# Kernel optimization log

Measured on AMD Instinct MI355X. Metric: run time of the kernel, lower is better.

Reference implementation:

```python
import jax, jax.numpy as jnp
import numpy as np

B, L, DIM, H, D, WS = 2, 2048, 1024, 16, 64, 256
SCALE = D ** -0.5


def _rope_tables(seq_len, dim, dtype):
    inv_freq = 1.0 / (10000.0 ** (jnp.arange(0, dim, 2, dtype=jnp.float32) / dim))
    t = jnp.arange(seq_len, dtype=jnp.float32)
    freqs = jnp.einsum('i,j->ij', t, inv_freq)          # [L, D/2]
    emb = jnp.concatenate([freqs, freqs], axis=-1)       # [L, D]
    return jnp.cos(emb).astype(dtype), jnp.sin(emb).astype(dtype)


def _rotate_half(x):
    x1, x2 = x[..., : x.shape[-1] // 2], x[..., x.shape[-1] // 2:]
    return jnp.concatenate([-x2, x1], axis=-1)


def _apply_rope(t, cos, sin):
    # t: [B, L, H, D]; cos/sin: [L, D] broadcast over batch and heads
    return t * cos[None, :, None, :] + _rotate_half(t) * sin[None, :, None, :]


def setup_inputs() -> dict:
    key = jax.random.key(0)
    k0, k1, k2 = jax.random.split(key, 3)
    x = jax.random.normal(k0, (B, L, DIM), dtype=jnp.float32)
    Wqkv = jax.random.normal(k1, (3 * H * D, DIM), dtype=jnp.float32) * 0.02
    bqkv = jnp.zeros((3 * H * D,), dtype=jnp.float32)
    Wproj = jax.random.normal(k2, (DIM, H * D), dtype=jnp.float32) * 0.02
    bproj = jnp.zeros((DIM,), dtype=jnp.float32)
    return {"x": x, "Wqkv": Wqkv, "bqkv": bqkv, "Wproj": Wproj, "bproj": bproj, "is_global": 1}


def _attention(x, Wqkv, bqkv, Wproj, bproj, is_global):
    b, l, _ = x.shape
    qkv = x @ Wqkv.T + bqkv                              # [B, L, 3*H*D]
    q, k, v = jnp.split(qkv, 3, axis=-1)
    q, k, v = (t.reshape(b, l, H, D) for t in (q, k, v))
    cos, sin = _rope_tables(l, D, x.dtype)
    q = _apply_rope(q, cos, sin)
    k = _apply_rope(k, cos, sin)
    if is_global:
        attn = jnp.einsum('bshd,bthd->bhst', q, k) * SCALE
        attn = jax.nn.softmax(attn, axis=-1)
        out = jnp.einsum('bhst,bthd->bshd', attn, v)     # [B, L, H, D]
    else:
        pad = (WS - l % WS) % WS
        if pad > 0:
            q, k, v = (jnp.pad(t, ((0, 0), (0, pad), (0, 0), (0, 0))) for t in (q, k, v))
        w = (l + pad) // WS
        q = q.reshape(b, w, WS, H, D)
        k = k.reshape(b, w, WS, H, D)
        v = v.reshape(b, w, WS, H, D)
        attn = jnp.einsum('bwshd,bwthd->bwhst', q, k) * SCALE
        attn = jax.nn.softmax(attn, axis=-1)
        out = jnp.einsum('bwhst,bwthd->bwshd', attn, v).reshape(b, w * WS, H, D)
        out = out[:, :l]
    return out.reshape(b, l, H * D) @ Wproj.T + bproj


def reference(x, Wqkv, bqkv, Wproj, bproj, is_global):
    return _attention(x, Wqkv, bqkv, Wproj, bproj, is_global)
```

## Files before the change

### kernel.cpp

```cpp
#include <hip/hip_runtime.h>
#include <math.h>

#define NB 2
#define NL 2048
#define NDIM 1024
#define NH 16
#define ND 64
#define NWS 256
#define NM (NB*NL)
#define QSCALE 0.18033688011112042f

typedef __attribute__((ext_vector_type(8))) short short8;
typedef __attribute__((ext_vector_type(4))) float f32x4;
typedef unsigned short ushort_t;
typedef unsigned int uint_t;

#define MFMA16(a,b,acc) __builtin_amdgcn_mfma_f32_16x16x32_bf16((a),(b),(acc),0,0,0)

static __device__ __forceinline__ ushort_t f2bf(float x){
    uint_t u = __float_as_uint(x);
    uint_t r = (u + 0x7fff + ((u >> 16) & 1)) >> 16;
    return (ushort_t)r;
}
static __device__ __forceinline__ float bf2f(ushort_t u){
    return __uint_as_float(((uint_t)u) << 16);
}
static __device__ __forceinline__ float fast_exp2(float x){
#if __has_builtin(__builtin_amdgcn_exp2f)
    return __builtin_amdgcn_exp2f(x);
#else
    return exp2f(x);
#endif
}

static __device__ __forceinline__ void async_load16(const void* g, void* l){
    __builtin_amdgcn_global_load_lds(
        (const __attribute__((address_space(1))) unsigned int*)g,
        (__attribute__((address_space(3))) unsigned int*)l, 16, 0, 0);
}

__launch_bounds__(256)
__global__ void split_all(const float* __restrict__ x,  ushort_t* __restrict__ xh,  ushort_t* __restrict__ xl,
                          const float* __restrict__ wq, ushort_t* __restrict__ wqh, ushort_t* __restrict__ wql,
                          const float* __restrict__ wp, ushort_t* __restrict__ wph, ushort_t* __restrict__ wpl)
{
    int i = blockIdx.x*256 + threadIdx.x;
    const float* in; ushort_t *oh, *ol;
    if (i < 1048576)      { in = x;  oh = xh;  ol = xl;  }
    else if (i < 1835008) { in = wq; oh = wqh; ol = wql; i -= 1048576; }
    else                  { in = wp; oh = wph; ol = wpl; i -= 1835008; }
    const int e = i*4;
    const float4 v = *(const float4*)(in + e);
    ushort_t h0=f2bf(v.x), h1=f2bf(v.y), h2=f2bf(v.z), h3=f2bf(v.w);
    ushort4 h4; h4.x=h0; h4.y=h1; h4.z=h2; h4.w=h3;
    ushort4 l4;
    l4.x=f2bf(v.x - bf2f(h0)); l4.y=f2bf(v.y - bf2f(h1));
    l4.z=f2bf(v.z - bf2f(h2)); l4.w=f2bf(v.w - bf2f(h3));
    *(ushort4*)(oh + e) = h4;
    *(ushort4*)(ol + e) = l4;
}

__launch_bounds__(256)
__global__ void rope_tab(float* __restrict__ tc, float* __restrict__ ts)
{
    const int idx = blockIdx.x*256 + threadIdx.x;
    const int j = idx >> 11, l = idx & (NL-1);
    const float invf = 1.0f / powf(10000.0f, (float)j * (1.0f/32.0f));
    float s, c;
    sincosf((float)l * invf, &s, &c);
    tc[idx] = c; ts[idx] = s;
}

template<int MODE>
__launch_bounds__(256, 3)
__global__ void gemm_hl(const ushort_t* __restrict__ Ah, const ushort_t* __restrict__ Al,
                        const ushort_t* __restrict__ Bh, const ushort_t* __restrict__ Bl,
                        const float* __restrict__ bias,
                        float* __restrict__ Cout,
                        ushort_t* __restrict__ oQh, ushort_t* __restrict__ oKh,
                        ushort_t* __restrict__ oVth,
                        const float* __restrict__ tcos, const float* __restrict__ tsin)
{
    __shared__ __align__(16) char smem[50176];
    ushort_t* sA_h = (ushort_t*)smem;
    ushort_t* sA_l = (ushort_t*)(smem + 8192);
    ushort_t* sB_h = (ushort_t*)(smem + 16384);
    ushort_t* sB_l = (ushort_t*)(smem + 20480);
    ushort_t* sBounce = (ushort_t*)smem;
    const int ebuf = 12288;
    const int bbuf = 24576;
    const int NTILE = (MODE==0) ? 128 : 64;
    const int WN    = (MODE==0) ? 64  : 32;
    const int NTT   = (MODE==0) ? 4   : 2;

    const int tid  = threadIdx.x;
    const int wv   = tid >> 6, lane = tid & 63;
    const int quad = lane >> 4, l16 = lane & 15;
    const int m0 = blockIdx.y << 7, n0 = blockIdx.x * NTILE;
    const int wr = wv >> 1, wc = wv & 1;

    const ushort_t* gsrc;
    ushort_t* lds_base;
    int rowb, npass;
    if (MODE == 1) {
        gsrc = (wv==0)?Ah:(wv==1)?Al:(wv==2)?Bh:Bl;
        lds_base = (wv==0)?sA_h:(wv==1)?sA_l:(wv==2)?sB_h:sB_l;
        rowb = (wv < 2) ? m0 : n0;
        npass = (wv < 2) ? 8 : 4;
    } else {
        if (wv == 0)      { gsrc = Ah; lds_base = sA_h; rowb = m0; npass = 8; }
        else if (wv == 1) { gsrc = Al; lds_base = sA_l; rowb = m0; npass = 8; }
        else { gsrc = Bh; lds_base = sB_h + (wv-2)*64*32; rowb = n0 + (wv-2)*64; npass = 4; }
    }
    const int rl = lane >> 2;
    const int cp = lane & 3;
    const int cg = cp ^ ((rl >> 1) & 3);
    const ushort_t* gptr = gsrc + (size_t)(rowb + rl)*NDIM + cg*8;

    f32x4 acc[4][NTT];
    #pragma unroll
    for (int i=0;i<4;++i)
        #pragma unroll
        for (int j=0;j<NTT;++j) acc[i][j] = (f32x4){0.f,0.f,0.f,0.f};

    const int swz = (l16 >> 1) & 3;
    const int ac_off = (wr*64 + l16)*32 + ((quad ^ swz) << 3);
    const int bc_off = (wc*WN + l16)*32 + ((quad ^ swz) << 3);

#define GSTAGE(BUF, KOFF) do { \
        const ushort_t* gp_ = gptr + (KOFF); \
        for (int p=0; p<npass; ++p) \
            async_load16(gp_ + (size_t)p*16*NDIM, (char*)lds_base + (BUF)*bbuf + p*1024); \
    } while(0)

#define GCOMP(BUF) do { \
        const int eo_ = (BUF)*ebuf; \
        short8 ah[4], al[4], bh[NTT], bl[NTT]; \
        _Pragma("unroll") \
        for (int t=0;t<4;++t){ \
            ah[t] = *(const short8*)&sA_h[eo_ + t*512 + ac_off]; \
            al[t] = *(const short8*)&sA_l[eo_ + t*512 + ac_off]; \
        } \
        _Pragma("unroll") \
        for (int t=0;t<NTT;++t){ \
            bh[t] = *(const short8*)&sB_h[eo_ + t*512 + bc_off]; \
            if (MODE == 1) bl[t] = *(const short8*)&sB_l[eo_ + t*512 + bc_off]; \
        } \
        _Pragma("unroll") \
        for (int mt=0;mt<4;++mt) \
            _Pragma("unroll") \
            for (int nt=0;nt<NTT;++nt){ \
                f32x4 a_ = acc[mt][nt]; \
                a_ = MFMA16(ah[mt], bh[nt], a_); \
                a_ = MFMA16(al[mt], bh[nt], a_); \
                if (MODE == 1) a_ = MFMA16(ah[mt], bl[nt], a_); \
                acc[mt][nt] = a_; \
            } \
    } while(0)

    GSTAGE(0, 0);
    for (int k0 = 0; k0 < NDIM; k0 += 64) {
        __syncthreads();
        GSTAGE(1, k0 + 32);
        GCOMP(0);
        __syncthreads();
        if (k0 + 64 < NDIM) GSTAGE(0, k0 + 64);
        GCOMP(1);
    }
#undef GSTAGE
#undef GCOMP

    if (MODE == 1) {
        const int colb = n0 + wc*32;
        float bq[2];
        #pragma unroll
        for (int nt=0;nt<2;++nt) bq[nt] = bias[colb + nt*16 + l16];
        #pragma unroll
        for (int mt=0;mt<4;++mt)
            #pragma unroll
            for (int r=0;r<4;++r){
                const int m = m0 + wr*64 + mt*16 + quad*4 + r;
                float* orow = Cout + (size_t)m*NDIM + colb;
                #pragma unroll
                for (int nt=0;nt<2;++nt)
                    orow[nt*16 + l16] = acc[mt][nt][r] + bq[nt];
            }
    } else {
        const int colb = n0 + wc*64;
        const int sel  = colb >> 10;
        const int head = (colb & 1023) >> 6;
        float bq[4];
        #pragma unroll
        for (int nt=0;nt<4;++nt) bq[nt] = bias[colb + nt*16 + l16];

        if (sel == 2) {
            __syncthreads();
            const int bb = m0 >> 11;
            const int Lb = (m0 & (NL-1)) + wr*64;
            ushort_t* sT = sBounce + wv*(64*72);
            const size_t gb = ((size_t)(bb*NH + head)*ND)*NL + Lb;
            const int drow = lane >> 3, dcol = lane & 7;
            #pragma unroll
            for (int mt=0;mt<4;++mt)
                #pragma unroll
                for (int nt=0;nt<4;++nt)
                    #pragma unroll
                    for (int r=0;r<4;++r)
                        sT[(nt*16+l16)*72 + mt*16 + quad*4 + r] = f2bf(acc[mt][nt][r] + bq[nt]);
            #pragma unroll
            for (int dd=0; dd<8; ++dd){
                const int d = dd*8 + drow;
                const uint4 v = *(const uint4*)&sT[d*72 + dcol*8];
                *(uint4*)(oVth + gb + (size_t)d*NL + dcol*8) = v;
            }
        } else {
            ushort_t* dh = sel ? oKh : oQh;
            const float qs = sel ? 1.0f : QSCALE;
            #pragma unroll
            for (int mt=0;mt<4;++mt)
                #pragma unroll
                for (int r=0;r<4;++r){
                    const int m = m0 + wr*64 + mt*16 + quad*4 + r;
                    const int bb = m >> 11, l = m & (NL-1);
                    const size_t ro = ((size_t)((bb*NH + head)*NL + l)) << 6;
                    #pragma unroll
                    for (int ntp=0;ntp<2;++ntp){
                        const int j = ntp*16 + l16;
                        const float c = tcos[j*NL + l];
                        const float s = tsin[j*NL + l];
                        const float x1 = acc[mt][ntp  ][r] + bq[ntp];
                        const float x2 = acc[mt][ntp+2][r] + bq[ntp+2];
                        const int d1 = ntp*16 + l16;
                        dh[ro + d1]      = f2bf((x1*c - x2*s) * qs);
                        dh[ro + d1 + 32] = f2bf((x2*c + x1*s) * qs);
                    }
                }
        }
    }
}

__launch_bounds__(256, 4)
__global__ void attn_mfma(const ushort_t* __restrict__ Qh,
                          const ushort_t* __restrict__ Kh,
                          const ushort_t* __restrict__ Vth,
                          ushort_t* __restrict__ AOh, ushort_t* __restrict__ AOl,
                          const int* __restrict__ isg)
{
    __shared__ __align__(16) char smem[40960];

    const int tid  = threadIdx.x;
    const int wv   = tid >> 6, lane = tid & 63;
    const int quad = lane >> 4, l16 = lane & 15;
    const int bh = blockIdx.x & 31, qt = blockIdx.x >> 5;
    const int q0w = qt*64 + wv*16;

    short8 bq0, bq1;
    {
        const size_t rb = (((size_t)bh*NL + q0w) << 6) + (size_t)(l16 << 6) + quad*8;
        bq0 = *(const short8*)(Qh + rb);
        bq1 = *(const short8*)(Qh + rb + 32);
    }
    short8 ones;
    #pragma unroll
    for (int j=0;j<8;++j) ones[j] = (short)0x3F80;

    f32x4 o[4];
    #pragma unroll
    for (int dnt=0; dnt<4; ++dnt) o[dnt] = (f32x4){0.f,0.f,0.f,0.f};
    f32x4 lsacc = (f32x4){0.f,0.f,0.f,0.f};

    const int gflag = isg[0];
    int klo, khi;
    if (gflag) { klo = 0; khi = NL; }
    else       { klo = (qt >> 2)*NWS; khi = klo + NWS; }

    const int swz4 = (l16 & 7) << 4;
    const int KC0 = l16*128 + (( quad*16      ) ^ swz4);
    const int KC1 = l16*128 + (( quad*16 + 64 ) ^ swz4);
    const int sPb = 32768 + wv*2048;
    int PW[4];
    #pragma unroll
    for (int knt=0; knt<4; ++knt)
        PW[knt] = sPb + l16*128 + ((knt*32 + quad*8) ^ swz4);
    const int PR0 = sPb + KC0;
    const int PR1 = sPb + KC1;

    const int r8  = lane >> 3;
    const int c8s = (lane & 7) ^ r8;
    const ushort_t* Kp = Kh + (((size_t)bh*NL) << 6)
                       + (size_t)(klo + wv*16 + r8)*64 + c8s*8;
    const ushort_t* Vp = Vth + (size_t)bh*ND*NL
                       + (size_t)(wv*16 + r8)*NL + klo + c8s*8;
    const int kdst = wv*2048;
    const int vdst = 16384 + wv*2048;

#define STAGE(BUF) do { \
        async_load16(Kp,          smem + (BUF)*8192 + kdst); \
        async_load16(Kp + 512,    smem + (BUF)*8192 + kdst + 1024); \
        async_load16(Vp,          smem + (BUF)*8192 + vdst); \
        async_load16(Vp + 8*NL,   smem + (BUF)*8192 + vdst + 1024); \
        Kp += 64*64; Vp += 64; } while (0)

#define TILE(BUF) do { \
        const char* kb_ = smem + (BUF)*8192; \
        const char* vb_ = smem + 16384 + (BUF)*8192; \
        f32x4 s_[4]; \
        _Pragma("unroll") \
        for (int knt=0; knt<4; ++knt) { \
            const short8 a0 = *(const short8*)(kb_ + knt*2048 + KC0); \
            const short8 a1 = *(const short8*)(kb_ + knt*2048 + KC1); \
            f32x4 t = (f32x4){0.f,0.f,0.f,0.f}; \
            t = MFMA16(a0, bq0, t); \
            t = MFMA16(a1, bq1, t); \
            s_[knt] = t; \
        } \
        _Pragma("unroll") \
        for (int knt=0; knt<4; ++knt) { \
            const uint_t u0 = __float_as_uint(fast_exp2(s_[knt][0])); \
            const uint_t u1 = __float_as_uint(fast_exp2(s_[knt][1])); \
            const uint_t u2 = __float_as_uint(fast_exp2(s_[knt][2])); \
            const uint_t u3 = __float_as_uint(fast_exp2(s_[knt][3])); \
            uint2 pk_; \
            pk_.x = __builtin_amdgcn_perm(u1, u0, 0x07060302u); \
            pk_.y = __builtin_amdgcn_perm(u3, u2, 0x07060302u); \
            *(uint2*)(smem + PW[knt]) = pk_; \
        } \
        const short8 fp0 = *(const short8*)(smem + PR0); \
        const short8 fp1 = *(const short8*)(smem + PR1); \
        lsacc = MFMA16(fp0, ones, lsacc); \
        lsacc = MFMA16(fp1, ones, lsacc); \
        _Pragma("unroll") \
        for (int dnt=0; dnt<4; ++dnt) { \
            const short8 v0 = *(const short8*)(vb_ + dnt*2048 + KC0); \
            const short8 v1 = *(const short8*)(vb_ + dnt*2048 + KC1); \
            f32x4 t = o[dnt]; \
            t = MFMA16(fp0, v0, t); \
            t = MFMA16(fp1, v1, t); \
            o[dnt] = t; \
        } } while (0)

    STAGE(0);
    for (int kt = klo; kt < khi; kt += 128) {
        __syncthreads();
        if (kt + 64 < khi) STAGE(1);
        TILE(0);
        __syncthreads();
        if (kt + 128 < khi) STAGE(0);
        TILE(1);
    }
#undef STAGE
#undef TILE

    const int bb = bh >> 4, hh = bh & 15;
    #pragma unroll
    for (int r=0; r<4; ++r) {
        const float inv = 1.0f / lsacc[r];
        const int row = q0w + quad*4 + r;
        const size_t ob = (((size_t)(bb*NL + row)) << 10) + (hh << 6);
        #pragma unroll
        for (int dnt=0; dnt<4; ++dnt) {
            const float val = o[dnt][r] * inv;
            const ushort_t h = f2bf(val);
            AOh[ob + dnt*16 + l16] = h;
            AOl[ob + dnt*16 + l16] = f2bf(val - bf2f(h));
        }
    }
}

extern "C" void kernel_launch(void* const* d_in, const int* in_sizes, int n_in,
                              void* d_out, int out_size, void* d_ws, size_t ws_size,
                              hipStream_t stream)
{
    const float* x     = (const float*)d_in[0];
    const float* Wqkv  = (const float*)d_in[1];
    const float* bqkv  = (const float*)d_in[2];
    const float* Wproj = (const float*)d_in[3];
    const float* bproj = (const float*)d_in[4];
    const int*   isg   = (const int*)d_in[5];
    float* out = (float*)d_out;
    char* base = (char*)d_ws;

    const size_t MB = 1024*1024;
    ushort_t* Qh  = (ushort_t*)(base);
    ushort_t* Kh  = (ushort_t*)(base + 16*MB);
    ushort_t* Vth = (ushort_t*)(base + 32*MB);
    ushort_t* xh  = (ushort_t*)(base + 48*MB);
    ushort_t* xl  = (ushort_t*)(base + 56*MB);
    ushort_t* AOh = xh;
    ushort_t* AOl = xl;
    ushort_t* Wqh = (ushort_t*)(base + 64*MB);
    ushort_t* Wql = (ushort_t*)(base + 64*MB + 6291456);
    ushort_t* Wph = (ushort_t*)(base + 76*MB);
    ushort_t* Wpl = (ushort_t*)(base + 76*MB + 2097152);
    float*    tcs = (float*)(base + 80*MB);
    float*    tsn = (float*)(base + 80*MB + 262144);

    split_all<<<8192, 256, 0, stream>>>(x, xh, xl, Wqkv, Wqh, Wql, Wproj, Wph, Wpl);
    rope_tab<<<256, 256, 0, stream>>>(tcs, tsn);

    gemm_hl<0><<<dim3(3*NDIM/128, NM/128), 256, 0, stream>>>(
        xh, xl, Wqh, Wql, bqkv, nullptr,
        Qh, Kh, Vth, tcs, tsn);

    attn_mfma<<<NB*NH*(NL/64), 256, 0, stream>>>(
        Qh, Kh, Vth, AOh, AOl, isg);

    gemm_hl<1><<<dim3(NDIM/64, NM/128), 256, 0, stream>>>(
        AOh, AOl, Wph, Wpl, bproj, out,
        nullptr, nullptr, nullptr, nullptr, nullptr);
}
```

Measured before the change: 231.0 us.

## Triple-buffer GEMM K-loop with balanced per-wave async loads and explicit waitcnt

Replaces the double-buffered K loop with a three-slot pipeline that keeps two stages of global-to-LDS loads in flight, using explicit vmcnt waits and raw s_barrier with sched barriers. Load work is redistributed so every wave issues the same number of async loads instead of some waves loading 8 rows and others 4. LDS grows to hold three slots and the occupancy hint drops from 3 to 2 blocks per CU, trading occupancy for deeper latency hiding.

```diff
diff --git a/kernel.cpp b/kernel.cpp
--- a/kernel.cpp
+++ b/kernel.cpp
@@ -72,7 +72,7 @@
 }
 
 template<int MODE>
-__launch_bounds__(256, 3)
+__launch_bounds__(256, 2)
 __global__ void gemm_hl(const ushort_t* __restrict__ Ah, const ushort_t* __restrict__ Al,
                         const ushort_t* __restrict__ Bh, const ushort_t* __restrict__ Bl,
                         const float* __restrict__ bias,
@@ -81,7 +81,7 @@
                         ushort_t* __restrict__ oVth,
                         const float* __restrict__ tcos, const float* __restrict__ tsin)
 {
-    __shared__ __align__(16) char smem[50176];
+    __shared__ __align__(16) char smem[74752];
     ushort_t* sA_h = (ushort_t*)smem;
     ushort_t* sA_l = (ushort_t*)(smem + 8192);
     ushort_t* sB_h = (ushort_t*)(smem + 16384);
@@ -89,33 +89,28 @@
     ushort_t* sBounce = (ushort_t*)smem;
     const int ebuf = 12288;
     const int bbuf = 24576;
-    const int NTILE = (MODE==0) ? 128 : 64;
-    const int WN    = (MODE==0) ? 64  : 32;
-    const int NTT   = (MODE==0) ? 4   : 2;
+    const int NTT  = (MODE==0) ? 4 : 2;
+    const int WN   = (MODE==0) ? 64 : 32;
 
     const int tid  = threadIdx.x;
     const int wv   = tid >> 6, lane = tid & 63;
     const int quad = lane >> 4, l16 = lane & 15;
-    const int m0 = blockIdx.y << 7, n0 = blockIdx.x * NTILE;
+    const int m0 = blockIdx.y << 7, n0 = blockIdx.x * ((MODE==0) ? 128 : 64);
     const int wr = wv >> 1, wc = wv & 1;
 
-    const ushort_t* gsrc;
-    ushort_t* lds_base;
-    int rowb, npass;
-    if (MODE == 1) {
-        gsrc = (wv==0)?Ah:(wv==1)?Al:(wv==2)?Bh:Bl;
-        lds_base = (wv==0)?sA_h:(wv==1)?sA_l:(wv==2)?sB_h:sB_l;
-        rowb = (wv < 2) ? m0 : n0;
-        npass = (wv < 2) ? 8 : 4;
-    } else {
-        if (wv == 0)      { gsrc = Ah; lds_base = sA_h; rowb = m0; npass = 8; }
-        else if (wv == 1) { gsrc = Al; lds_base = sA_l; rowb = m0; npass = 8; }
-        else { gsrc = Bh; lds_base = sB_h + (wv-2)*64*32; rowb = n0 + (wv-2)*64; npass = 4; }
-    }
     const int rl = lane >> 2;
     const int cp = lane & 3;
     const int cg = cp ^ ((rl >> 1) & 3);
-    const ushort_t* gptr = gsrc + (size_t)(rowb + rl)*NDIM + cg*8;
+    const ushort_t* pAh = Ah + (size_t)(m0 + 32*wv + rl)*NDIM + cg*8;
+    const ushort_t* pAl = Al + (size_t)(m0 + 32*wv + rl)*NDIM + cg*8;
+    const ushort_t* pBh;
+    const ushort_t* pBl;
+    if (MODE == 0) { pBh = Bh + (size_t)(n0 + 32*wv + rl)*NDIM + cg*8; pBl = pBh; }
+    else { pBh = Bh + (size_t)(n0 + 16*wv + rl)*NDIM + cg*8;
+           pBl = Bl + (size_t)(n0 + 16*wv + rl)*NDIM + cg*8; }
+    char* dA  = smem + wv*2048;
+    char* dB0 = smem + 16384 + ((MODE==0) ? wv*2048 : wv*1024);
+    char* dB1 = smem + 20480 + wv*1024;
 
     f32x4 acc[4][NTT];
     #pragma unroll
@@ -127,14 +122,23 @@
     const int ac_off = (wr*64 + l16)*32 + ((quad ^ swz) << 3);
     const int bc_off = (wc*WN + l16)*32 + ((quad ^ swz) << 3);
 
-#define GSTAGE(BUF, KOFF) do { \
-        const ushort_t* gp_ = gptr + (KOFF); \
-        for (int p=0; p<npass; ++p) \
-            async_load16(gp_ + (size_t)p*16*NDIM, (char*)lds_base + (BUF)*bbuf + p*1024); \
+#define GSTAGE(SLOT, KOFF) do { \
+        const int so_ = (SLOT)*bbuf; \
+        async_load16(pAh + (KOFF),           dA + so_); \
+        async_load16(pAh + 16*NDIM + (KOFF), dA + so_ + 1024); \
+        async_load16(pAl + (KOFF),           dA + so_ + 8192); \
+        async_load16(pAl + 16*NDIM + (KOFF), dA + so_ + 9216); \
+        if (MODE == 0) { \
+            async_load16(pBh + (KOFF),           dB0 + so_); \
+            async_load16(pBh + 16*NDIM + (KOFF), dB0 + so_ + 1024); \
+        } else { \
+            async_load16(pBh + (KOFF), dB0 + so_); \
+            async_load16(pBl + (KOFF), dB1 + so_); \
+        } \
     } while(0)
 
-#define GCOMP(BUF) do { \
-        const int eo_ = (BUF)*ebuf; \
+#define GCOMP(SLOT) do { \
+        const int eo_ = (SLOT)*ebuf; \
         short8 ah[4], al[4], bh[NTT], bl[NTT]; \
         _Pragma("unroll") \
         for (int t=0;t<4;++t){ \
@@ -158,17 +162,30 @@
             } \
     } while(0)
 
-    GSTAGE(0, 0);
-    for (int k0 = 0; k0 < NDIM; k0 += 64) {
-        __syncthreads();
-        GSTAGE(1, k0 + 32);
-        GCOMP(0);
-        __syncthreads();
-        if (k0 + 64 < NDIM) GSTAGE(0, k0 + 64);
-        GCOMP(1);
+#define GPHASE(SLOT, K0, VN) do { \
+        asm volatile("s_waitcnt vmcnt(" #VN ")" ::: "memory"); \
+        __builtin_amdgcn_sched_barrier(0); \
+        __builtin_amdgcn_s_barrier(); \
+        __builtin_amdgcn_sched_barrier(0); \
+        GCOMP(SLOT); \
+        asm volatile("s_waitcnt lgkmcnt(0)" ::: "memory"); \
+        __builtin_amdgcn_sched_barrier(0); \
+        __builtin_amdgcn_s_barrier(); \
+        __builtin_amdgcn_sched_barrier(0); \
+        if ((K0) + 96 < NDIM) GSTAGE(SLOT, (K0) + 96); \
+    } while(0)
+
+    GSTAGE(0, 0); GSTAGE(1, 32); GSTAGE(2, 64);
+    for (int k0 = 0; k0 < 960; k0 += 96) {
+        GPHASE(0, k0,      12);
+        GPHASE(1, k0 + 32, 12);
+        GPHASE(2, k0 + 64, 12);
     }
+    GPHASE(0, 960, 0);
+    GPHASE(1, 992, 0);
 #undef GSTAGE
 #undef GCOMP
+#undef GPHASE
 
     if (MODE == 1) {
         const int colb = n0 + wc*32;
```

Result: no change. 226.5 us (-1.9%).
